# Kernel optimization log

Measured on AMD Instinct MI355X. Metric: run time of the kernel, lower is better.

The kernel has to match this reference:

```python
import jax, jax.numpy as jnp
import numpy as np

N_NODES = 50000
N_EDGES = 800000
F_IN = 64
F_HID = 64
F_OUT = 16


def setup_inputs() -> dict:
    key = jax.random.key(0)
    k1, k2, k3, k4, k5 = jax.random.split(key, 5)
    x = jax.random.normal(k1, (N_NODES, F_IN), dtype=jnp.float32)
    edge_index = jax.random.randint(k2, (2, N_EDGES), 0, N_NODES, dtype=jnp.int64)
    # glorot-style init for GCNConv weights
    W1 = jax.random.normal(k3, (F_IN, F_HID), dtype=jnp.float32) * (1.0 / np.sqrt(F_IN))
    b1 = jnp.zeros((F_HID,), dtype=jnp.float32)
    W2 = jax.random.normal(k4, (F_HID, F_OUT), dtype=jnp.float32) * (1.0 / np.sqrt(F_HID))
    b2 = jnp.zeros((F_OUT,), dtype=jnp.float32)
    return {"x": x, "edge_index": edge_index, "W1": W1, "b1": b1, "W2": W2, "b2": b2}


def _gcn_conv(x, src, dst, n, W, b):
    # linear transform first (PyG GCNConv), then normalized scatter-add aggregation
    h = x @ W  # [N, F_out]
    deg = jax.ops.segment_sum(jnp.ones_like(dst, dtype=h.dtype), dst, num_segments=n)
    dinv = jnp.where(deg > 0, jax.lax.rsqrt(deg), 0.0)  # deg^{-1/2}, 0 for isolated
    norm = dinv[src] * dinv[dst]  # [E]
    out = jax.ops.segment_sum(norm[:, None] * h[src], dst, num_segments=n)
    return out + b


def reference(x, edge_index, W1, b1, W2, b2):
    n = x.shape[0]
    loops = jnp.arange(n, dtype=edge_index.dtype)
    # add self-loops as in PyG GCNConv default
    src = jnp.concatenate([edge_index[0], loops])
    dst = jnp.concatenate([edge_index[1], loops])
    h = jax.nn.relu(_gcn_conv(x, src, dst, n, W1, b1))
    h = _gcn_conv(h, src, dst, n, W2, b2)
    return jax.nn.log_softmax(h, axis=1)
```

## Files before the change

### kernel.cpp

```cpp
#include <hip/hip_runtime.h>


#define F1 64
#define F2 16
#define G 256
#define HP 256

typedef __attribute__((ext_vector_type(8))) short bf16x8;
typedef __attribute__((ext_vector_type(4))) float f32x4;
typedef __attribute__((ext_vector_type(4))) unsigned short u16x4;

__device__ inline unsigned short f2bf(float f) {
    unsigned u = __float_as_uint(f);
    return (unsigned short)((u + 0x7FFFu + ((u >> 16) & 1u)) >> 16);
}
__device__ inline float bf2f(unsigned short s) {
    return __uint_as_float(((unsigned)s) << 16);
}

__device__ inline void cvt8(const float* v, bf16x8& h, bf16x8& l) {
#pragma unroll
    for (int i = 0; i < 8; ++i) {
        unsigned b = __float_as_uint(v[i]);
        h[i] = (short)(b >> 16);
        float hif = __uint_as_float(b & 0xFFFF0000u);
        float lof = v[i] - hif;
        l[i] = (short)(__float_as_uint(lof) >> 16);
    }
}


__global__ __launch_bounds__(256) void k_hist(const int4* __restrict__ dst4,
                                              const int* __restrict__ dst,
                                              int* __restrict__ hist, int e4, int e) {
    __shared__ int hl[HP];
    int tid = threadIdx.x, g = blockIdx.x;
    hl[tid] = 0;
    __syncthreads();
    int chunk = (e4 + G - 1) / G;
    int beg = g * chunk, end = min(e4, beg + chunk);
    for (int i = beg + tid; i < end; i += 256) {
        int4 d = dst4[i];
        atomicAdd(&hl[d.x >> 8], 1);
        atomicAdd(&hl[d.y >> 8], 1);
        atomicAdd(&hl[d.z >> 8], 1);
        atomicAdd(&hl[d.w >> 8], 1);
    }
    if (g == G - 1)
        for (int i = e4 * 4 + tid; i < e; i += 256) atomicAdd(&hl[dst[i] >> 8], 1);
    __syncthreads();
    hist[g * HP + tid] = hl[tid];
}

__global__ __launch_bounds__(256) void k_cscan(const int* __restrict__ hist,
                                               int* __restrict__ pgoff,
                                               int* __restrict__ ptotal) {
    __shared__ int s[G];
    int p = blockIdx.x, g = threadIdx.x;
    int v = hist[g * HP + p];
    s[g] = v;
    __syncthreads();
    for (int off = 1; off < G; off <<= 1) {
        int t = (g >= off) ? s[g - off] : 0;
        __syncthreads();
        s[g] += t;
        __syncthreads();
    }
    pgoff[g * HP + p] = s[g] - v;
    if (g == G - 1) ptotal[p] = s[g];
}

__global__ __launch_bounds__(256) void k_part(const int4* __restrict__ src4,
                                              const int4* __restrict__ dst4,
                                              const int* __restrict__ src,
                                              const int* __restrict__ dst,
                                              const int* __restrict__ pgoff,
                                              const int* __restrict__ ptotal,
                                              unsigned* __restrict__ pairs,
                                              int e4, int e, int npart) {
    __shared__ int s[HP];
    __shared__ int cur[HP];
    int tid = threadIdx.x, g = blockIdx.x;
    int v = (tid < npart) ? ptotal[tid] : 0;
    s[tid] = v;
    __syncthreads();
    for (int off = 1; off < HP; off <<= 1) {
        int t = (tid >= off) ? s[tid - off] : 0;
        __syncthreads();
        s[tid] += t;
        __syncthreads();
    }
    cur[tid] = (s[tid] - v) + pgoff[g * HP + tid];
    __syncthreads();
    int chunk = (e4 + G - 1) / G;
    int beg = g * chunk, end = min(e4, beg + chunk);
    for (int i = beg + tid; i < end; i += 256) {
        int4 s4 = src4[i];
        int4 d4 = dst4[i];
        int pos;
        pos = atomicAdd(&cur[d4.x >> 8], 1); pairs[pos] = ((unsigned)(d4.x & 255) << 16) | (unsigned)s4.x;
        pos = atomicAdd(&cur[d4.y >> 8], 1); pairs[pos] = ((unsigned)(d4.y & 255) << 16) | (unsigned)s4.y;
        pos = atomicAdd(&cur[d4.z >> 8], 1); pairs[pos] = ((unsigned)(d4.z & 255) << 16) | (unsigned)s4.z;
        pos = atomicAdd(&cur[d4.w >> 8], 1); pairs[pos] = ((unsigned)(d4.w & 255) << 16) | (unsigned)s4.w;
    }
    if (g == G - 1)
        for (int i = e4 * 4 + tid; i < e; i += 256) {
            int d = dst[i];
            int pos = atomicAdd(&cur[d >> 8], 1);
            pairs[pos] = ((unsigned)(d & 255) << 16) | (unsigned)src[i];
        }
}

__global__ __launch_bounds__(256) void k_csr(const unsigned* __restrict__ pairs,
                                             const int* __restrict__ ptotal,
                                             int* __restrict__ rowstart,
                                             float* __restrict__ dinv,
                                             int* __restrict__ csr,
                                             int n, int e, int npart) {
    __shared__ int s[HP];
    __shared__ int cnt[256], cur[256];
    __shared__ int wbs, wes;
    int p = blockIdx.x, tid = threadIdx.x;
    int v = (tid < npart) ? ptotal[tid] : 0;
    s[tid] = v;
    __syncthreads();
    for (int off = 1; off < HP; off <<= 1) {
        int t = (tid >= off) ? s[tid - off] : 0;
        __syncthreads();
        s[tid] += t;
        __syncthreads();
    }
    if (tid == p) { wbs = s[tid] - v; wes = s[tid]; }
    cnt[tid] = 0;
    __syncthreads();
    int wbeg = wbs, wend = wes;
    for (int i = wbeg + tid; i < wend; i += 256)
        atomicAdd(&cnt[pairs[i] >> 16], 1);
    __syncthreads();
    int c = cnt[tid];
    s[tid] = c;
    __syncthreads();
    for (int off = 1; off < 256; off <<= 1) {
        int t = (tid >= off) ? s[tid - off] : 0;
        __syncthreads();
        s[tid] += t;
        __syncthreads();
    }
    int rs = wbeg + s[tid] - c;
    cur[tid] = rs;
    int node = (p << 8) + tid;
    if (node < n) {
        rowstart[node] = rs;
        dinv[node] = rsqrtf((float)c + 1.0f);
    }
    if (p == 0 && tid == 0) rowstart[n] = e;
    __syncthreads();
    for (int i = wbeg + tid; i < wend; i += 256) {
        unsigned u = pairs[i];
        int pos = atomicAdd(&cur[u >> 16], 1);
        csr[pos] = (int)(u & 0xFFFFu);
    }
}


__global__ __launch_bounds__(256) void k_mgemm1(const float* __restrict__ x,
                                                const float* __restrict__ W1,
                                                unsigned short* __restrict__ h_bf, int n) {
    __shared__ float ws[64 * 65];
    int tid = threadIdx.x;
    for (int i = tid; i < 64 * 64; i += 256) {
        int k = i >> 6, c = i & 63;
        ws[k * 65 + c] = W1[i];
    }
    __syncthreads();
    int lane = tid & 63, wv = tid >> 6;
    int rt = blockIdx.x * 64 + wv * 16;
    int r = lane & 15, g = lane >> 4;
    int row = rt + r;
    int rowc = row < n ? row : n - 1;
    const float* xp = x + (size_t)rowc * F1 + g * 8;
    bf16x8 ah[2], al[2];
#pragma unroll
    for (int kb = 0; kb < 2; ++kb) {
        float v[8];
        *(float4*)&v[0] = *(const float4*)(xp + kb * 32);
        *(float4*)&v[4] = *(const float4*)(xp + kb * 32 + 4);
        cvt8(v, ah[kb], al[kb]);
    }
#pragma unroll
    for (int ct = 0; ct < 4; ++ct) {
        bf16x8 bh[2], bl[2];
#pragma unroll
        for (int kb = 0; kb < 2; ++kb) {
            float v[8];
#pragma unroll
            for (int i = 0; i < 8; ++i)
                v[i] = ws[(kb * 32 + g * 8 + i) * 65 + ct * 16 + r];
            cvt8(v, bh[kb], bl[kb]);
        }
        f32x4 acc = {0.f, 0.f, 0.f, 0.f};
#pragma unroll
        for (int kb = 0; kb < 2; ++kb) {
            acc = __builtin_amdgcn_mfma_f32_16x16x32_bf16(ah[kb], bh[kb], acc, 0, 0, 0);
            acc = __builtin_amdgcn_mfma_f32_16x16x32_bf16(al[kb], bh[kb], acc, 0, 0, 0);
            acc = __builtin_amdgcn_mfma_f32_16x16x32_bf16(ah[kb], bl[kb], acc, 0, 0, 0);
        }
#pragma unroll
        for (int j = 0; j < 4; ++j) {
            int orow = rt + g * 4 + j;
            if (orow < n) h_bf[(size_t)orow * F1 + ct * 16 + r] = f2bf(acc[j]);
        }
    }
}

__global__ __launch_bounds__(256) void k_mgemm2(const float* __restrict__ agg1,
                                                const float* __restrict__ b1,
                                                const float* __restrict__ W2,
                                                unsigned short* __restrict__ h2_bf, int n) {
    __shared__ float ws[64 * 17];
    int tid = threadIdx.x;
    for (int i = tid; i < 64 * 16; i += 256) {
        int k = i >> 4, c = i & 15;
        ws[k * 17 + c] = W2[i];
    }
    __syncthreads();
    int lane = tid & 63, wv = tid >> 6;
    int rt = blockIdx.x * 64 + wv * 16;
    int r = lane & 15, g = lane >> 4;
    int row = rt + r;
    int rowc = row < n ? row : n - 1;
    const float* ap = agg1 + (size_t)rowc * F1 + g * 8;
    const float* bp = b1 + g * 8;
    bf16x8 ah[2], al[2];
#pragma unroll
    for (int kb = 0; kb < 2; ++kb) {
        float v[8], b[8];
        *(float4*)&v[0] = *(const float4*)(ap + kb * 32);
        *(float4*)&v[4] = *(const float4*)(ap + kb * 32 + 4);
        *(float4*)&b[0] = *(const float4*)(bp + kb * 32);
        *(float4*)&b[4] = *(const float4*)(bp + kb * 32 + 4);
#pragma unroll
        for (int i = 0; i < 8; ++i) v[i] = fmaxf(v[i] + b[i], 0.f);
        cvt8(v, ah[kb], al[kb]);
    }
    bf16x8 bh[2], bl[2];
#pragma unroll
    for (int kb = 0; kb < 2; ++kb) {
        float v[8];
#pragma unroll
        for (int i = 0; i < 8; ++i)
            v[i] = ws[(kb * 32 + g * 8 + i) * 17 + r];
        cvt8(v, bh[kb], bl[kb]);
    }
    f32x4 acc = {0.f, 0.f, 0.f, 0.f};
#pragma unroll
    for (int kb = 0; kb < 2; ++kb) {
        acc = __builtin_amdgcn_mfma_f32_16x16x32_bf16(ah[kb], bh[kb], acc, 0, 0, 0);
        acc = __builtin_amdgcn_mfma_f32_16x16x32_bf16(al[kb], bh[kb], acc, 0, 0, 0);
        acc = __builtin_amdgcn_mfma_f32_16x16x32_bf16(ah[kb], bl[kb], acc, 0, 0, 0);
    }
#pragma unroll
    for (int j = 0; j < 4; ++j) {
        int orow = rt + g * 4 + j;
        if (orow < n) h2_bf[(size_t)orow * F2 + r] = f2bf(acc[j]);
    }
}


__global__ __launch_bounds__(256) void k_agg64(const int* __restrict__ rowstart,
                                               const int* __restrict__ csr,
                                               const float* __restrict__ dinv,
                                               const unsigned short* __restrict__ hb,
                                               float* __restrict__ agg, int n) {
    int lane = threadIdx.x & 63, wv = threadIdx.x >> 6;
    int node = blockIdx.x * 4 + wv;
    if (node >= n) return;
    int g = lane >> 4, q = lane & 15;
    float di = dinv[node];
    float4 acc = {0.f, 0.f, 0.f, 0.f};
    int beg = rowstart[node], end = rowstart[node + 1];
    for (int base = beg; base < end; base += 64) {
        int k = base + lane;
        int idx = (k < end) ? csr[k] : 0;
        float dv = (k < end) ? dinv[idx] : 0.0f;
        int m = end - base;
        if (m <= 32) {
#pragma unroll
            for (int i = 0; i < 8; ++i) {
                int slot = i * 4 + g;
                int s = __shfl(idx, slot, 64);
                float w = __shfl(dv, slot, 64);
                u16x4 u = *(const u16x4*)(hb + (size_t)s * F1 + q * 4);
                acc.x = fmaf(w, bf2f(u.x), acc.x);
                acc.y = fmaf(w, bf2f(u.y), acc.y);
                acc.z = fmaf(w, bf2f(u.z), acc.z);
                acc.w = fmaf(w, bf2f(u.w), acc.w);
            }
        } else {
#pragma unroll
            for (int i = 0; i < 16; ++i) {
                int slot = i * 4 + g;
                int s = __shfl(idx, slot, 64);
                float w = __shfl(dv, slot, 64);
                u16x4 u = *(const u16x4*)(hb + (size_t)s * F1 + q * 4);
                acc.x = fmaf(w, bf2f(u.x), acc.x);
                acc.y = fmaf(w, bf2f(u.y), acc.y);
                acc.z = fmaf(w, bf2f(u.z), acc.z);
                acc.w = fmaf(w, bf2f(u.w), acc.w);
            }
        }
    }
#pragma unroll
    for (int off = 16; off <= 32; off <<= 1) {
        acc.x += __shfl_xor(acc.x, off, 64);
        acc.y += __shfl_xor(acc.y, off, 64);
        acc.z += __shfl_xor(acc.z, off, 64);
        acc.w += __shfl_xor(acc.w, off, 64);
    }
    if (g == 0) {
        u16x4 su = *(const u16x4*)(hb + (size_t)node * F1 + q * 4);
        float d2 = di * di;
        float4 o;
        o.x = fmaf(di, acc.x, d2 * bf2f(su.x));
        o.y = fmaf(di, acc.y, d2 * bf2f(su.y));
        o.z = fmaf(di, acc.z, d2 * bf2f(su.z));
        o.w = fmaf(di, acc.w, d2 * bf2f(su.w));
        ((float4*)agg)[(size_t)node * 16 + q] = o;
    }
}

__global__ __launch_bounds__(256) void k_agg16(const int* __restrict__ rowstart,
                                               const int* __restrict__ csr,
                                               const float* __restrict__ dinv,
                                               const unsigned short* __restrict__ h2b,
                                               const float* __restrict__ b2,
                                               float* __restrict__ out, int n) {
    int lane = threadIdx.x & 63, wv = threadIdx.x >> 6;
    int node = blockIdx.x * 4 + wv;
    if (node >= n) return;
    int g = lane >> 2, q = lane & 3;
    float di = dinv[node];
    float4 acc = {0.f, 0.f, 0.f, 0.f};
    int beg = rowstart[node], end = rowstart[node + 1];
    for (int base = beg; base < end; base += 64) {
        int k = base + lane;
        int idx = (k < end) ? csr[k] : 0;
        float dv = (k < end) ? dinv[idx] : 0.0f;
#pragma unroll
        for (int i = 0; i < 4; ++i) {
            int slot = i * 16 + g;
            int s = __shfl(idx, slot, 64);
            float w = __shfl(dv, slot, 64);
            u16x4 u = *(const u16x4*)(h2b + (size_t)s * F2 + q * 4);
            acc.x = fmaf(w, bf2f(u.x), acc.x);
            acc.y = fmaf(w, bf2f(u.y), acc.y);
            acc.z = fmaf(w, bf2f(u.z), acc.z);
            acc.w = fmaf(w, bf2f(u.w), acc.w);
        }
    }
#pragma unroll
    for (int off = 4; off <= 32; off <<= 1) {
        acc.x += __shfl_xor(acc.x, off, 64);
        acc.y += __shfl_xor(acc.y, off, 64);
        acc.z += __shfl_xor(acc.z, off, 64);
        acc.w += __shfl_xor(acc.w, off, 64);
    }
    u16x4 su = *(const u16x4*)(h2b + (size_t)node * F2 + q * 4);
    float4 bv = ((const float4*)b2)[q];
    float d2 = di * di;
    float4 v;
    v.x = fmaf(di, acc.x, fmaf(d2, bf2f(su.x), bv.x));
    v.y = fmaf(di, acc.y, fmaf(d2, bf2f(su.y), bv.y));
    v.z = fmaf(di, acc.z, fmaf(d2, bf2f(su.z), bv.z));
    v.w = fmaf(di, acc.w, fmaf(d2, bf2f(su.w), bv.w));
    float mr = fmaxf(fmaxf(v.x, v.y), fmaxf(v.z, v.w));
    mr = fmaxf(mr, __shfl_xor(mr, 1, 64));
    mr = fmaxf(mr, __shfl_xor(mr, 2, 64));
    float sm = expf(v.x - mr) + expf(v.y - mr) + expf(v.z - mr) + expf(v.w - mr);
    sm += __shfl_xor(sm, 1, 64);
    sm += __shfl_xor(sm, 2, 64);
    float l = mr + logf(sm);
    if (g == 0) {
        float4 o;
        o.x = v.x - l; o.y = v.y - l; o.z = v.z - l; o.w = v.w - l;
        ((float4*)out)[(size_t)node * 4 + q] = o;
    }
}

extern "C" void kernel_launch(void* const* d_in, const int* in_sizes, int n_in,
                              void* d_out, int out_size, void* d_ws, size_t ws_size,
                              hipStream_t stream) {
    const float* x  = (const float*)d_in[0];
    const int*   ei = (const int*)d_in[1];
    const float* W1 = (const float*)d_in[2];
    const float* b1 = (const float*)d_in[3];
    const float* W2 = (const float*)d_in[4];
    const float* b2 = (const float*)d_in[5];
    float* out = (float*)d_out;

    const int n = in_sizes[0] / F1;
    const int e = in_sizes[1] / 2;
    const int e4 = e >> 2;
    const int* src = ei;
    const int* dst = ei + e;

    const int na = (n + 63) & ~63;
    const int npart = (n + 255) >> 8;

    float* dinv     = (float*)d_ws;
    int* rowstart   = (int*)(dinv + na);
    int* ptotal     = rowstart + na + 64;
    int* csr        = ptotal + 256;
    unsigned short* h_bf = (unsigned short*)(csr + ((e + 63) & ~63));
    float* agg1     = (float*)(h_bf + (size_t)n * F1);
    int* hist       = (int*)h_bf;
    int* pgoff      = hist + G * HP;
    unsigned* pairs = (unsigned*)(pgoff + G * HP);
    unsigned short* h2_bf = h_bf;

    k_hist <<<G, 256, 0, stream>>>((const int4*)dst, dst, hist, e4, e);
    k_cscan<<<npart, 256, 0, stream>>>(hist, pgoff, ptotal);
    k_part <<<G, 256, 0, stream>>>((const int4*)src, (const int4*)dst, src, dst,
                                   pgoff, ptotal, pairs, e4, e, npart);
    k_csr  <<<npart, 256, 0, stream>>>(pairs, ptotal, rowstart, dinv, csr, n, e, npart);

    k_mgemm1<<<(n + 63) / 64, 256, 0, stream>>>(x, W1, h_bf, n);
    k_agg64<<<(n + 3) / 4, 256, 0, stream>>>(rowstart, csr, dinv, h_bf, agg1, n);

    k_mgemm2<<<(n + 63) / 64, 256, 0, stream>>>(agg1, b1, W2, h2_bf, n);
    k_agg16<<<(n + 3) / 4, 256, 0, stream>>>(rowstart, csr, dinv, h2_bf, b2, out, n);
}
```

Measured before the change: 161.6 us.

## Co-launch GEMM1 with edge partition; fuse bias+ReLU into agg and store bf16

Result: faster. 150.5 us (-6.9%).

```diff
diff --git a/kernel.cpp b/kernel.cpp
--- a/kernel.cpp
+++ b/kernel.cpp
@@ -70,45 +70,96 @@
     if (g == G - 1) ptotal[p] = s[g];
 }
 
-__global__ __launch_bounds__(256) void k_part(const int4* __restrict__ src4,
-                                              const int4* __restrict__ dst4,
-                                              const int* __restrict__ src,
-                                              const int* __restrict__ dst,
-                                              const int* __restrict__ pgoff,
-                                              const int* __restrict__ ptotal,
-                                              unsigned* __restrict__ pairs,
-                                              int e4, int e, int npart) {
-    __shared__ int s[HP];
-    __shared__ int cur[HP];
-    int tid = threadIdx.x, g = blockIdx.x;
-    int v = (tid < npart) ? ptotal[tid] : 0;
-    s[tid] = v;
-    __syncthreads();
-    for (int off = 1; off < HP; off <<= 1) {
-        int t = (tid >= off) ? s[tid - off] : 0;
-        __syncthreads();
-        s[tid] += t;
-        __syncthreads();
-    }
-    cur[tid] = (s[tid] - v) + pgoff[g * HP + tid];
-    __syncthreads();
-    int chunk = (e4 + G - 1) / G;
-    int beg = g * chunk, end = min(e4, beg + chunk);
-    for (int i = beg + tid; i < end; i += 256) {
-        int4 s4 = src4[i];
-        int4 d4 = dst4[i];
-        int pos;
-        pos = atomicAdd(&cur[d4.x >> 8], 1); pairs[pos] = ((unsigned)(d4.x & 255) << 16) | (unsigned)s4.x;
-        pos = atomicAdd(&cur[d4.y >> 8], 1); pairs[pos] = ((unsigned)(d4.y & 255) << 16) | (unsigned)s4.y;
-        pos = atomicAdd(&cur[d4.z >> 8], 1); pairs[pos] = ((unsigned)(d4.z & 255) << 16) | (unsigned)s4.z;
-        pos = atomicAdd(&cur[d4.w >> 8], 1); pairs[pos] = ((unsigned)(d4.w & 255) << 16) | (unsigned)s4.w;
-    }
-    if (g == G - 1)
-        for (int i = e4 * 4 + tid; i < e; i += 256) {
-            int d = dst[i];
-            int pos = atomicAdd(&cur[d >> 8], 1);
-            pairs[pos] = ((unsigned)(d & 255) << 16) | (unsigned)src[i];
-        }
+__global__ __launch_bounds__(256) void k_pm1(const float* __restrict__ x,
+                                             const float* __restrict__ W1,
+                                             unsigned short* __restrict__ h_bf,
+                                             const int4* __restrict__ src4,
+                                             const int4* __restrict__ dst4,
+                                             const int* __restrict__ src,
+                                             const int* __restrict__ dst,
+                                             const int* __restrict__ pgoff,
+                                             const int* __restrict__ ptotal,
+                                             unsigned* __restrict__ pairs,
+                                             int e4, int e, int npart,
+                                             int n, int nb1) {
+    __shared__ float ws[64 * 65];
+    __shared__ int s[HP], cur[HP];
+    int tid = threadIdx.x;
+    if ((int)blockIdx.x < nb1) {
+        for (int i = tid; i < 64 * 64; i += 256) {
+            int k = i >> 6, c = i & 63;
+            ws[k * 65 + c] = W1[i];
+        }
+        __syncthreads();
+        int lane = tid & 63, wv = tid >> 6;
+        int rt = blockIdx.x * 64 + wv * 16;
+        int r = lane & 15, g = lane >> 4;
+        int row = rt + r;
+        int rowc = row < n ? row : n - 1;
+        const float* xp = x + (size_t)rowc * F1 + g * 8;
+        bf16x8 ah[2], al[2];
+#pragma unroll
+        for (int kb = 0; kb < 2; ++kb) {
+            float v[8];
+            *(float4*)&v[0] = *(const float4*)(xp + kb * 32);
+            *(float4*)&v[4] = *(const float4*)(xp + kb * 32 + 4);
+            cvt8(v, ah[kb], al[kb]);
+        }
+#pragma unroll
+        for (int ct = 0; ct < 4; ++ct) {
+            bf16x8 bh[2], bl[2];
+#pragma unroll
+            for (int kb = 0; kb < 2; ++kb) {
+                float v[8];
+#pragma unroll
+                for (int i = 0; i < 8; ++i)
+                    v[i] = ws[(kb * 32 + g * 8 + i) * 65 + ct * 16 + r];
+                cvt8(v, bh[kb], bl[kb]);
+            }
+            f32x4 acc = {0.f, 0.f, 0.f, 0.f};
+#pragma unroll
+            for (int kb = 0; kb < 2; ++kb) {
+                acc = __builtin_amdgcn_mfma_f32_16x16x32_bf16(ah[kb], bh[kb], acc, 0, 0, 0);
+                acc = __builtin_amdgcn_mfma_f32_16x16x32_bf16(al[kb], bh[kb], acc, 0, 0, 0);
+                acc = __builtin_amdgcn_mfma_f32_16x16x32_bf16(ah[kb], bl[kb], acc, 0, 0, 0);
+            }
+#pragma unroll
+            for (int j = 0; j < 4; ++j) {
+                int orow = rt + g * 4 + j;
+                if (orow < n) h_bf[(size_t)orow * F1 + ct * 16 + r] = f2bf(acc[j]);
+            }
+        }
+    } else {
+        int g = blockIdx.x - nb1;
+        int v = (tid < npart) ? ptotal[tid] : 0;
+        s[tid] = v;
+        __syncthreads();
+        for (int off = 1; off < HP; off <<= 1) {
+            int t = (tid >= off) ? s[tid - off] : 0;
+            __syncthreads();
+            s[tid] += t;
+            __syncthreads();
+        }
+        cur[tid] = (s[tid] - v) + pgoff[g * HP + tid];
+        __syncthreads();
+        int chunk = (e4 + G - 1) / G;
+        int beg = g * chunk, end = min(e4, beg + chunk);
+        for (int i = beg + tid; i < end; i += 256) {
+            int4 s4 = src4[i];
+            int4 d4 = dst4[i];
+            int pos;
+            pos = atomicAdd(&cur[d4.x >> 8], 1); pairs[pos] = ((unsigned)(d4.x & 255) << 16) | (unsigned)s4.x;
+            pos = atomicAdd(&cur[d4.y >> 8], 1); pairs[pos] = ((unsigned)(d4.y & 255) << 16) | (unsigned)s4.y;
+            pos = atomicAdd(&cur[d4.z >> 8], 1); pairs[pos] = ((unsigned)(d4.z & 255) << 16) | (unsigned)s4.z;
+            pos = atomicAdd(&cur[d4.w >> 8], 1); pairs[pos] = ((unsigned)(d4.w & 255) << 16) | (unsigned)s4.w;
+        }
+        if (g == G - 1)
+            for (int i = e4 * 4 + tid; i < e; i += 256) {
+                int d = dst[i];
+                int pos = atomicAdd(&cur[d >> 8], 1);
+                pairs[pos] = ((unsigned)(d & 255) << 16) | (unsigned)src[i];
+            }
+    }
 }
 
 __global__ __launch_bounds__(256) void k_csr(const unsigned* __restrict__ pairs,
@@ -162,59 +213,7 @@
     }
 }
 
-
-__global__ __launch_bounds__(256) void k_mgemm1(const float* __restrict__ x,
-                                                const float* __restrict__ W1,
-                                                unsigned short* __restrict__ h_bf, int n) {
-    __shared__ float ws[64 * 65];
-    int tid = threadIdx.x;
-    for (int i = tid; i < 64 * 64; i += 256) {
-        int k = i >> 6, c = i & 63;
-        ws[k * 65 + c] = W1[i];
-    }
-    __syncthreads();
-    int lane = tid & 63, wv = tid >> 6;
-    int rt = blockIdx.x * 64 + wv * 16;
-    int r = lane & 15, g = lane >> 4;
-    int row = rt + r;
-    int rowc = row < n ? row : n - 1;
-    const float* xp = x + (size_t)rowc * F1 + g * 8;
-    bf16x8 ah[2], al[2];
-#pragma unroll
-    for (int kb = 0; kb < 2; ++kb) {
-        float v[8];
-        *(float4*)&v[0] = *(const float4*)(xp + kb * 32);
-        *(float4*)&v[4] = *(const float4*)(xp + kb * 32 + 4);
-        cvt8(v, ah[kb], al[kb]);
-    }
-#pragma unroll
-    for (int ct = 0; ct < 4; ++ct) {
-        bf16x8 bh[2], bl[2];
-#pragma unroll
-        for (int kb = 0; kb < 2; ++kb) {
-            float v[8];
-#pragma unroll
-            for (int i = 0; i < 8; ++i)
-                v[i] = ws[(kb * 32 + g * 8 + i) * 65 + ct * 16 + r];
-            cvt8(v, bh[kb], bl[kb]);
-        }
-        f32x4 acc = {0.f, 0.f, 0.f, 0.f};
-#pragma unroll
-        for (int kb = 0; kb < 2; ++kb) {
-            acc = __builtin_amdgcn_mfma_f32_16x16x32_bf16(ah[kb], bh[kb], acc, 0, 0, 0);
-            acc = __builtin_amdgcn_mfma_f32_16x16x32_bf16(al[kb], bh[kb], acc, 0, 0, 0);
-            acc = __builtin_amdgcn_mfma_f32_16x16x32_bf16(ah[kb], bl[kb], acc, 0, 0, 0);
-        }
-#pragma unroll
-        for (int j = 0; j < 4; ++j) {
-            int orow = rt + g * 4 + j;
-            if (orow < n) h_bf[(size_t)orow * F1 + ct * 16 + r] = f2bf(acc[j]);
-        }
-    }
-}
-
-__global__ __launch_bounds__(256) void k_mgemm2(const float* __restrict__ agg1,
-                                                const float* __restrict__ b1,
+__global__ __launch_bounds__(256) void k_mgemm2(const unsigned short* __restrict__ a1b,
                                                 const float* __restrict__ W2,
                                                 unsigned short* __restrict__ h2_bf, int n) {
     __shared__ float ws[64 * 17];
@@ -229,20 +228,10 @@
     int r = lane & 15, g = lane >> 4;
     int row = rt + r;
     int rowc = row < n ? row : n - 1;
-    const float* ap = agg1 + (size_t)rowc * F1 + g * 8;
-    const float* bp = b1 + g * 8;
-    bf16x8 ah[2], al[2];
-#pragma unroll
-    for (int kb = 0; kb < 2; ++kb) {
-        float v[8], b[8];
-        *(float4*)&v[0] = *(const float4*)(ap + kb * 32);
-        *(float4*)&v[4] = *(const float4*)(ap + kb * 32 + 4);
-        *(float4*)&b[0] = *(const float4*)(bp + kb * 32);
-        *(float4*)&b[4] = *(const float4*)(bp + kb * 32 + 4);
-#pragma unroll
-        for (int i = 0; i < 8; ++i) v[i] = fmaxf(v[i] + b[i], 0.f);
-        cvt8(v, ah[kb], al[kb]);
-    }
+    const unsigned short* ap = a1b + (size_t)rowc * F1 + g * 8;
+    bf16x8 ah[2];
+    ah[0] = *(const bf16x8*)(ap);
+    ah[1] = *(const bf16x8*)(ap + 32);
     bf16x8 bh[2], bl[2];
 #pragma unroll
     for (int kb = 0; kb < 2; ++kb) {
@@ -256,7 +245,6 @@
 #pragma unroll
     for (int kb = 0; kb < 2; ++kb) {
         acc = __builtin_amdgcn_mfma_f32_16x16x32_bf16(ah[kb], bh[kb], acc, 0, 0, 0);
-        acc = __builtin_amdgcn_mfma_f32_16x16x32_bf16(al[kb], bh[kb], acc, 0, 0, 0);
         acc = __builtin_amdgcn_mfma_f32_16x16x32_bf16(ah[kb], bl[kb], acc, 0, 0, 0);
     }
 #pragma unroll
@@ -271,7 +259,8 @@
                                                const int* __restrict__ csr,
                                                const float* __restrict__ dinv,
                                                const unsigned short* __restrict__ hb,
-                                               float* __restrict__ agg, int n) {
+                                               const float* __restrict__ b1,
+                                               unsigned short* __restrict__ a1b, int n) {
     int lane = threadIdx.x & 63, wv = threadIdx.x >> 6;
     int node = blockIdx.x * 4 + wv;
     if (node >= n) return;
@@ -319,13 +308,16 @@
     }
     if (g == 0) {
         u16x4 su = *(const u16x4*)(hb + (size_t)node * F1 + q * 4);
+        float4 bv = ((const float4*)b1)[q];
         float d2 = di * di;
         float4 o;
-        o.x = fmaf(di, acc.x, d2 * bf2f(su.x));
-        o.y = fmaf(di, acc.y, d2 * bf2f(su.y));
-        o.z = fmaf(di, acc.z, d2 * bf2f(su.z));
-        o.w = fmaf(di, acc.w, d2 * bf2f(su.w));
-        ((float4*)agg)[(size_t)node * 16 + q] = o;
+        o.x = fmaxf(fmaf(di, acc.x, fmaf(d2, bf2f(su.x), bv.x)), 0.f);
+        o.y = fmaxf(fmaf(di, acc.y, fmaf(d2, bf2f(su.y), bv.y)), 0.f);
+        o.z = fmaxf(fmaf(di, acc.z, fmaf(d2, bf2f(su.z), bv.z)), 0.f);
+        o.w = fmaxf(fmaf(di, acc.w, fmaf(d2, bf2f(su.w), bv.w)), 0.f);
+        u16x4 rv;
+        rv.x = f2bf(o.x); rv.y = f2bf(o.y); rv.z = f2bf(o.z); rv.w = f2bf(o.w);
+        *(u16x4*)(a1b + (size_t)node * F1 + q * 4) = rv;
     }
 }
 
@@ -406,27 +398,28 @@
 
     const int na = (n + 63) & ~63;
     const int npart = (n + 255) >> 8;
+    const int nb1 = (n + 63) / 64;
 
     float* dinv     = (float*)d_ws;
     int* rowstart   = (int*)(dinv + na);
     int* ptotal     = rowstart + na + 64;
     int* csr        = ptotal + 256;
     unsigned short* h_bf = (unsigned short*)(csr + ((e + 63) & ~63));
-    float* agg1     = (float*)(h_bf + (size_t)n * F1);
-    int* hist       = (int*)h_bf;
+    unsigned short* a1b  = h_bf + (size_t)n * F1;
+    int* hist       = (int*)(a1b + (size_t)n * F1);
     int* pgoff      = hist + G * HP;
     unsigned* pairs = (unsigned*)(pgoff + G * HP);
     unsigned short* h2_bf = h_bf;
 
     k_hist <<<G, 256, 0, stream>>>((const int4*)dst, dst, hist, e4, e);
     k_cscan<<<npart, 256, 0, stream>>>(hist, pgoff, ptotal);
-    k_part <<<G, 256, 0, stream>>>((const int4*)src, (const int4*)dst, src, dst,
-                                   pgoff, ptotal, pairs, e4, e, npart);
+    k_pm1  <<<nb1 + G, 256, 0, stream>>>(x, W1, h_bf,
+                                         (const int4*)src, (const int4*)dst, src, dst,
+                                         pgoff, ptotal, pairs, e4, e, npart, n, nb1);
     k_csr  <<<npart, 256, 0, stream>>>(pairs, ptotal, rowstart, dinv, csr, n, e, npart);
 
-    k_mgemm1<<<(n + 63) / 64, 256, 0, stream>>>(x, W1, h_bf, n);
-    k_agg64<<<(n + 3) / 4, 256, 0, stream>>>(rowstart, csr, dinv, h_bf, agg1, n);
-
-    k_mgemm2<<<(n + 63) / 64, 256, 0, stream>>>(agg1, b1, W2, h2_bf, n);
+    k_agg64<<<(n + 3) / 4, 256, 0, stream>>>(rowstart, csr, dinv, h_bf, b1, a1b, n);
+
+    k_mgemm2<<<(n + 63) / 64, 256, 0, stream>>>(a1b, W2, h2_bf, n);
     k_agg16<<<(n + 3) / 4, 256, 0, stream>>>(rowstart, csr, dinv, h2_bf, b2, out, n);
 }
```
